# Kernel optimization log

Measured on AMD Instinct MI355X. Metric: run time of the kernel, lower is better.

Reference implementation:

```python
import jax, jax.numpy as jnp
import numpy as np

R = 32  # voxel resolution

def leaky(x):
    return jnp.where(x > 0, x, 0.1 * x)

def bn(x, gamma, beta, axes, eps=1e-4):
    mu = jnp.mean(x, axis=axes, keepdims=True)
    var = jnp.var(x, axis=axes, keepdims=True)
    shape = [1] * x.ndim
    shape[1] = x.shape[1]
    g = gamma.reshape(shape)
    b = beta.reshape(shape)
    return (x - mu) * jax.lax.rsqrt(var + eps) * g + b

def voxelize(features, coords, r):
    # features: (B, C, N), coords: (B, 3, N)
    B, C, N = features.shape
    mean = jnp.mean(coords, axis=2, keepdims=True)
    norm = (coords - mean + 1.0) / 2.0 * r
    norm = jnp.clip(norm, 0.0, r - 1.0)            # (B, 3, N) continuous voxel coords
    vox = jnp.round(norm).astype(jnp.int32)
    flat = (vox[:, 0] * r + vox[:, 1]) * r + vox[:, 2]      # (B, N)
    seg = (flat + jnp.arange(B, dtype=jnp.int32)[:, None] * (r ** 3)).reshape(-1)
    data = features.transpose(0, 2, 1).reshape(B * N, C)
    sums = jax.ops.segment_sum(data, seg, num_segments=B * r ** 3)
    cnt = jax.ops.segment_sum(jnp.ones((B * N,), data.dtype), seg, num_segments=B * r ** 3)
    avg = sums / jnp.maximum(cnt, 1.0)[:, None]
    grid = avg.reshape(B, r, r, r, C).transpose(0, 4, 1, 2, 3)  # (B, C, r, r, r)
    return grid, norm

def trilinear_devoxelize(grid, norm, r):
    # grid: (B, C, r, r, r), norm: (B, 3, N) in [0, r-1]
    B, C = grid.shape[:2]
    N = norm.shape[2]
    lo = jnp.floor(norm).astype(jnp.int32)
    frac = norm - lo.astype(norm.dtype)
    hi = jnp.minimum(lo + 1, r - 1)
    gf = grid.reshape(B, C, r ** 3)
    out = jnp.zeros((B, C, N), grid.dtype)
    for dx in (0, 1):
        for dy in (0, 1):
            for dz in (0, 1):
                ix = hi[:, 0] if dx else lo[:, 0]
                iy = hi[:, 1] if dy else lo[:, 1]
                iz = hi[:, 2] if dz else lo[:, 2]
                wx = frac[:, 0] if dx else 1.0 - frac[:, 0]
                wy = frac[:, 1] if dy else 1.0 - frac[:, 1]
                wz = frac[:, 2] if dz else 1.0 - frac[:, 2]
                idx = (ix * r + iy) * r + iz                    # (B, N)
                g = jnp.take_along_axis(gf, idx[:, None, :], axis=2)  # (B, C, N)
                out = out + g * (wx * wy * wz)[:, None, :]
    return out

def conv3d(x, w, b):
    y = jax.lax.conv_general_dilated(
        x, w, window_strides=(1, 1, 1), padding=[(1, 1)] * 3,
        dimension_numbers=('NCDHW', 'OIDHW', 'NCDHW'))
    return y + b[None, :, None, None, None]

def setup_inputs() -> dict:
    key = jax.random.key(0)
    ks = jax.random.split(key, 8)
    B, Cin, Cout, N = 8, 64, 64, 32768
    s1 = 1.0 / np.sqrt(Cin * 27)
    s2 = 1.0 / np.sqrt(Cout * 27)
    return {
        'features': jax.random.normal(ks[0], (B, Cin, N), jnp.float32),
        'coords': jax.random.normal(ks[1], (B, 3, N), jnp.float32),
        'conv1_w': jax.random.normal(ks[2], (Cout, Cin, 3, 3, 3), jnp.float32) * s1,
        'conv1_b': jnp.zeros((Cout,), jnp.float32),
        'bn1_g': jnp.ones((Cout,), jnp.float32),
        'bn1_b': jnp.zeros((Cout,), jnp.float32),
        'conv2_w': jax.random.normal(ks[3], (Cout, Cout, 3, 3, 3), jnp.float32) * s2,
        'conv2_b': jnp.zeros((Cout,), jnp.float32),
        'bn2_g': jnp.ones((Cout,), jnp.float32),
        'bn2_b': jnp.zeros((Cout,), jnp.float32),
        'mlp_w': jax.random.normal(ks[4], (Cout, Cin), jnp.float32) / np.sqrt(Cin),
        'mlp_b': jnp.zeros((Cout,), jnp.float32),
        'bnp_g': jnp.ones((Cout,), jnp.float32),
        'bnp_b': jnp.zeros((Cout,), jnp.float32),
    }

def reference(features, coords, conv1_w, conv1_b, bn1_g, bn1_b,
              conv2_w, conv2_b, bn2_g, bn2_b, mlp_w, mlp_b, bnp_g, bnp_b):
    grid, norm = voxelize(features, coords, R)
    v = leaky(bn(conv3d(grid, conv1_w, conv1_b), bn1_g, bn1_b, (0, 2, 3, 4)))
    v = leaky(bn(conv3d(v, conv2_w, conv2_b), bn2_g, bn2_b, (0, 2, 3, 4)))
    sampled = trilinear_devoxelize(v, norm, R)                 # (B, Cout, N)
    p = jnp.einsum('oi,bin->bon', mlp_w, features) + mlp_b[None, :, None]
    p = leaky(bn(p, bnp_g, bnp_b, (0, 2)))
    fused = sampled + p
    return fused, v
```

## Files before the change

### kernel.cpp

```cpp
#include <hip/hip_runtime.h>
#include <hip/hip_bf16.h>

#define BB 8
#define CC 64
#define NPTS 32768
#define RR 32
#define RV 32768
#define MTOT (BB*RV)
#define EPSV 1e-4f

#define OFF_BUFA 0u
#define OFF_BUFB 16777216u
#define OFF_WB1  25165824u
#define OFF_WB2  25221120u
#define OFF_ZG   25276416u
#define OFF_BASE 25276480u
#define OFF_AUX  25800768u
#define OFF_CELL 25801024u
#define OFF_CNT  26063168u
#define OFF_MEAN 26325312u
#define OFF_PART1 26325504u
#define OFF_PART2 26456576u
#define OFF_SCL1 26587648u
#define OFF_SFT1 26587712u
#define OFF_SCL2 26587776u
#define OFF_SFT2 26587840u
#define OFF_WM   26587904u
#define OFF_PARTP 26590208u
#define OFF_SCLP 27114496u
#define OFF_SFTP 27114560u
#define OFF_NORM 33554432u

typedef __attribute__((ext_vector_type(8))) __bf16 bf16x8;
typedef __attribute__((ext_vector_type(8))) unsigned short u16x8;
typedef __attribute__((ext_vector_type(4))) float f32x4;

__device__ __forceinline__ float b2f(ushort u) {
    union { unsigned u; float f; } x; x.u = ((unsigned)u) << 16; return x.f;
}
__device__ __forceinline__ ushort f2b(float f) {
    __hip_bfloat16 h = __float2bfloat16(f);
    return *reinterpret_cast<ushort*>(&h);
}

__global__ void k_coord_mean(const float* __restrict__ coords, float* __restrict__ mean) {
    int ba = blockIdx.x >> 3, ch = blockIdx.x & 7;
    const float* src = coords + (size_t)ba * NPTS + ch * 4096;
    float s = 0.f;
    for (int i = threadIdx.x; i < 4096; i += 256) s += src[i];
    __shared__ float red[256];
    red[threadIdx.x] = s; __syncthreads();
    for (int w = 128; w > 0; w >>= 1) {
        if (threadIdx.x < w) red[threadIdx.x] += red[threadIdx.x + w];
        __syncthreads();
    }
    if (threadIdx.x == 0) atomicAdd(&mean[ba], red[0]);
}

__global__ void k_cellid(const float* __restrict__ coords, const float* __restrict__ mean,
                         float* __restrict__ norm, int* __restrict__ cellid,
                         unsigned* __restrict__ cnt) {
    int idx = blockIdx.x * 256 + threadIdx.x;
    int b = idx >> 15, n = idx & (NPTS - 1);
    int flat = 0;
    #pragma unroll
    for (int a = 0; a < 3; ++a) {
        float c = coords[((size_t)(b * 3 + a)) * NPTS + n];
        float nm = (c - mean[b * 3 + a] * (1.0f / NPTS) + 1.0f) * (0.5f * RR);
        nm = fminf(fmaxf(nm, 0.0f), (float)(RR - 1));
        norm[((size_t)(b * 3 + a)) * NPTS + n] = nm;
        flat = flat * RR + (int)rintf(nm);
    }
    int cell = b * RV + flat;
    cellid[idx] = cell;
    atomicAdd(&cnt[cell], 1u);
}

__global__ void k_scan1(const unsigned* __restrict__ cnt, unsigned* __restrict__ base,
                        unsigned* __restrict__ aux) {
    int tid = threadIdx.x;
    int c0 = blockIdx.x * 1024 + tid * 4;
    unsigned v0 = cnt[c0], v1 = cnt[c0 + 1], v2 = cnt[c0 + 2], v3 = cnt[c0 + 3];
    unsigned tot = v0 + v1 + v2 + v3;
    __shared__ unsigned sc[256];
    sc[tid] = tot; __syncthreads();
    for (int off = 1; off < 256; off <<= 1) {
        unsigned t = (tid >= off) ? sc[tid - off] : 0u;
        __syncthreads();
        sc[tid] += t;
        __syncthreads();
    }
    unsigned excl = sc[tid] - tot;
    base[c0] = excl;
    base[c0 + 1] = excl + v0;
    base[c0 + 2] = excl + v0 + v1;
    base[c0 + 3] = excl + v0 + v1 + v2;
    if (tid == 255) aux[blockIdx.x] = sc[255];
}

__global__ void k_scan2(unsigned* __restrict__ aux) {
    int tid = threadIdx.x;
    unsigned own = aux[tid];
    __shared__ unsigned sc[256];
    sc[tid] = own; __syncthreads();
    for (int off = 1; off < 256; off <<= 1) {
        unsigned t = (tid >= off) ? sc[tid - off] : 0u;
        __syncthreads();
        sc[tid] += t;
        __syncthreads();
    }
    aux[tid] = sc[tid] - own;
}

__global__ void k_scan3(unsigned* __restrict__ base, const unsigned* __restrict__ aux) {
    int i = blockIdx.x * 256 + threadIdx.x;
    base[i] += aux[i >> 10];
}

__global__ __launch_bounds__(256) void k_scatfeat(
    const float* __restrict__ feats, const int* __restrict__ cellid,
    unsigned* __restrict__ base, ushort* __restrict__ fsort,
    const ushort* __restrict__ wmb, const float* __restrict__ mbias,
    ushort* __restrict__ pb, float* __restrict__ partp) {
    __shared__ float t[64 * 65];
    __shared__ unsigned spos[64];
    __shared__ float sf[512];
    int b = blockIdx.x >> 9;
    int n0 = (blockIdx.x & 511) * 64;
    int tid = threadIdx.x;
    #pragma unroll
    for (int k = 0; k < 4; ++k) {
        int li = k * 256 + tid;
        int c = li >> 4, n4 = (li & 15) * 4;
        float4 v = *reinterpret_cast<const float4*>(
            &feats[((size_t)(b * 64 + c)) * NPTS + n0 + n4]);
        t[c * 65 + n4 + 0] = v.x;
        t[c * 65 + n4 + 1] = v.y;
        t[c * 65 + n4 + 2] = v.z;
        t[c * 65 + n4 + 3] = v.w;
    }
    if (tid < 64) {
        int cell = cellid[(b << 15) + n0 + tid];
        spos[tid] = atomicAdd(&base[cell], 1u);
    }
    __syncthreads();
    #pragma unroll
    for (int it = 0; it < 2; ++it) {
        int pl = it * 32 + (tid >> 3);
        int j = tid & 7;
        unsigned pos = spos[pl];
        u16x8 v;
        #pragma unroll
        for (int k = 0; k < 8; ++k) v[k] = f2b(t[(j * 8 + k) * 65 + pl]);
        *reinterpret_cast<u16x8*>(fsort + (((size_t)pos) << 6) + j * 8) = v;
    }
    int w = tid >> 6, l = tid & 63;
    int nl = l & 15, kg = l >> 4;
    bf16x8 Af[2];
    #pragma unroll
    for (int ks = 0; ks < 2; ++ks) {
        union { u16x8 u; bf16x8 h; } cv;
        #pragma unroll
        for (int j = 0; j < 8; ++j)
            cv.u[j] = f2b(t[(ks * 32 + kg * 8 + j) * 65 + w * 16 + nl]);
        Af[ks] = cv.h;
    }
    f32x4 acc[4];
    #pragma unroll
    for (int cb = 0; cb < 4; ++cb) acc[cb] = (f32x4){0.f, 0.f, 0.f, 0.f};
    #pragma unroll
    for (int ks = 0; ks < 2; ++ks)
        #pragma unroll
        for (int cb = 0; cb < 4; ++cb) {
            bf16x8 Bf = *reinterpret_cast<const bf16x8*>(wmb + (cb * 16 + nl) * 64 + ks * 32 + kg * 8);
            acc[cb] = __builtin_amdgcn_mfma_f32_16x16x32_bf16(Af[ks], Bf, acc[cb], 0, 0, 0);
        }
    float ss[4] = {0.f, 0.f, 0.f, 0.f}, qq[4] = {0.f, 0.f, 0.f, 0.f};
    #pragma unroll
    for (int cb = 0; cb < 4; ++cb) {
        float bsv = mbias[cb * 16 + nl];
        #pragma unroll
        for (int r = 0; r < 4; ++r) {
            float yv = acc[cb][r] + bsv;
            int pt = w * 16 + kg * 4 + r;
            pb[(((size_t)((b << 15) + n0 + pt)) << 6) + cb * 16 + nl] = f2b(yv);
            ss[cb] += yv; qq[cb] += yv * yv;
        }
    }
    #pragma unroll
    for (int cb = 0; cb < 4; ++cb) {
        ss[cb] += __shfl_xor(ss[cb], 16); ss[cb] += __shfl_xor(ss[cb], 32);
        qq[cb] += __shfl_xor(qq[cb], 16); qq[cb] += __shfl_xor(qq[cb], 32);
    }
    if (l < 16) {
        #pragma unroll
        for (int cb = 0; cb < 4; ++cb) {
            sf[w * 128 + cb * 16 + nl] = ss[cb];
            sf[w * 128 + 64 + cb * 16 + nl] = qq[cb];
        }
    }
    __syncthreads();
    if (tid < 128)
        partp[(size_t)tid * 4096 + blockIdx.x] =
            sf[tid] + sf[128 + tid] + sf[256 + tid] + sf[384 + tid];
}

__global__ __launch_bounds__(256) void k_gather(
    const ushort* __restrict__ fsort, const unsigned* __restrict__ base,
    const unsigned* __restrict__ cnt, __hip_bfloat16* __restrict__ xb) {
    int cell = blockIdx.x * 4 + (threadIdx.x >> 6);
    int lane = threadIdx.x & 63;
    unsigned n = cnt[cell];
    unsigned start = base[cell] - n;
    const ushort* rows = fsort + (((size_t)start) << 6) + lane;
    float acc = 0.f;
    unsigned i = 0;
    for (; i + 8 <= n; i += 8) {
        float f0 = b2f(rows[((size_t)(i + 0)) << 6]);
        float f1 = b2f(rows[((size_t)(i + 1)) << 6]);
        float f2 = b2f(rows[((size_t)(i + 2)) << 6]);
        float f3 = b2f(rows[((size_t)(i + 3)) << 6]);
        float f4 = b2f(rows[((size_t)(i + 4)) << 6]);
        float f5 = b2f(rows[((size_t)(i + 5)) << 6]);
        float f6 = b2f(rows[((size_t)(i + 6)) << 6]);
        float f7 = b2f(rows[((size_t)(i + 7)) << 6]);
        acc += ((f0 + f1) + (f2 + f3)) + ((f4 + f5) + (f6 + f7));
    }
    for (; i < n; ++i) acc += b2f(rows[((size_t)i) << 6]);
    float inv = (n > 0) ? (1.0f / (float)n) : 0.f;
    xb[((size_t)cell << 6) + lane] = __float2bfloat16(acc * inv);
}

__global__ void k_wb(const float* __restrict__ w, __hip_bfloat16* __restrict__ wb) {
    int i = blockIdx.x * 256 + threadIdx.x;
    if (i >= CC * CC * 27) return;
    int tap = i % 27, t = i / 27;
    int ci = t & 63, co = t >> 6;
    int half = ci >> 5;
    wb[(((size_t)((half * 27 + tap) * 64 + co)) << 5) + (ci & 31)] = __float2bfloat16(w[i]);
}

__global__ void k_wm(const float* __restrict__ w, ushort* __restrict__ wmb) {
    int i = blockIdx.x * 256 + threadIdx.x;
    if (i < 4096) wmb[i] = f2b(w[i]);
}

template<int MODE>
__global__ __launch_bounds__(512, 4) void k_conv_mfma(
    const ushort* __restrict__ src, const ushort* __restrict__ wb,
    const float* __restrict__ bias, const float* __restrict__ scl,
    const float* __restrict__ sft, ushort* __restrict__ y,
    float* __restrict__ part, const ushort* __restrict__ zg) {
    __shared__ __align__(16) char sh[64000 + 16384];
    char* wsh = sh + 64000;
    int tid = threadIdx.x;
    int lane = tid & 63, wid = tid >> 6;
    int tile = ((blockIdx.x & 7) << 6) | (blockIdx.x >> 3);
    int twi = tile & 3, thi = (tile >> 2) & 3;
    int tdi = (tile >> 4) & 3, b = tile >> 6;
    int d0 = tdi * 8, h0 = thi * 8, w0 = twi * 8;

    auto stage_wgt = [&](int half, int g) {
        const ushort* wgrp = wb + (((half * 27 + g * 2)) << 11);
        char* wdst = wsh + (g & 1) * 8192;
        int c = (wid << 6) + lane;
        int row = c >> 2, off = c & 3;
        const ushort* gsrc = wgrp + (((row << 2) + (off ^ (row & 3))) << 3);
        __builtin_amdgcn_global_load_lds(
            (const __attribute__((address_space(1))) void*)gsrc,
            (__attribute__((address_space(3))) void*)(wdst + (wid << 10)), 16, 0, 0);
    };

    auto stage_halo = [&](int half) {
        float sc8[8], sf8[8];
        if (MODE == 1) {
            int c0 = half * 32 + (lane & 3) * 8;
            #pragma unroll
            for (int j = 0; j < 8; ++j) { sc8[j] = scl[c0 + j]; sf8[j] = sft[c0 + j]; }
        }
        #pragma unroll
        for (int it = 0; it < 8; ++it) {
            int idx = it * 8 + wid;
            int c = (idx << 6) + lane;
            if (c < 4000) {
                int row = c >> 2, off = c & 3;
                int dz = row / 100, rem = row - dz * 100;
                int hz = rem / 10, wz = rem - hz * 10;
                int gd = d0 - 1 + dz, gh = h0 - 1 + hz, gw = w0 - 1 + wz;
                bool inb = ((unsigned)gd < 32u) && ((unsigned)gh < 32u) && ((unsigned)gw < 32u);
                size_t vbase = (((size_t)((b << 15) | (gd << 10) | (gh << 5) | gw)) << 6) + half * 32;
                if (MODE == 0) {
                    int soff = off ^ (row & 3);
                    const ushort* gsrc = inb ? src + vbase + soff * 8 : zg;
                    __builtin_amdgcn_global_load_lds(
                        (const __attribute__((address_space(1))) void*)gsrc,
                        (__attribute__((address_space(3))) void*)(sh + (idx << 10)), 16, 0, 0);
                } else {
                    u16x8 v = {0, 0, 0, 0, 0, 0, 0, 0};
                    if (inb) {
                        v = *reinterpret_cast<const u16x8*>(src + vbase + off * 8);
                        #pragma unroll
                        for (int j = 0; j < 8; ++j) {
                            float f = fmaf(b2f(v[j]), sc8[j], sf8[j]);
                            f = f > 0.f ? f : 0.1f * f;
                            v[j] = f2b(f);
                        }
                    }
                    *reinterpret_cast<u16x8*>(sh + (row << 6) + ((off ^ (row & 3)) << 4)) = v;
                }
            }
        }
    };

    int nl = lane & 15, kg = lane >> 4;
    int rbase = wid * 100 + (nl >> 3) * 10 + (nl & 7);

    f32x4 acc[4][4];
    #pragma unroll
    for (int mi = 0; mi < 4; ++mi)
        #pragma unroll
        for (int cb = 0; cb < 4; ++cb) acc[mi][cb] = (f32x4){0.f, 0.f, 0.f, 0.f};

    auto compute = [&](int g) {
        const char* wlds = wsh + (g & 1) * 8192;
        #pragma unroll
        for (int tl = 0; tl < 2; ++tl) {
            int t = g * 2 + tl;
            if (t < 27) {
                int kd = t / 9, rm = t - kd * 9;
                int kh = rm / 3, kw = rm - kh * 3;
                int rt = rbase + kd * 100 + kh * 10 + kw;
                bf16x8 a[4];
                #pragma unroll
                for (int mi = 0; mi < 4; ++mi) {
                    int r = rt + mi * 20;
                    a[mi] = *reinterpret_cast<const bf16x8*>(
                        sh + (r << 6) + ((kg ^ (r & 3)) << 4));
                }
                bf16x8 bf[4];
                #pragma unroll
                for (int cb = 0; cb < 4; ++cb) {
                    int rowb = tl * 64 + cb * 16 + nl;
                    bf[cb] = *reinterpret_cast<const bf16x8*>(
                        wlds + (rowb << 6) + ((kg ^ (rowb & 3)) << 4));
                }
                __builtin_amdgcn_s_setprio(1);
                #pragma unroll
                for (int mi = 0; mi < 4; ++mi)
                    #pragma unroll
                    for (int cb = 0; cb < 4; ++cb)
                        acc[mi][cb] = __builtin_amdgcn_mfma_f32_16x16x32_bf16(
                            a[mi], bf[cb], acc[mi][cb], 0, 0, 0);
                __builtin_amdgcn_s_setprio(0);
            }
        }
    };

    stage_halo(0);
    stage_wgt(0, 0);
    __syncthreads();
    #pragma unroll 1
    for (int g = 0; g < 14; ++g) {
        if (g < 13) stage_wgt(0, g + 1);
        compute(g);
        __syncthreads();
    }
    stage_halo(1);
    stage_wgt(1, 0);
    __syncthreads();
    #pragma unroll 1
    for (int g = 0; g < 14; ++g) {
        if (g < 13) stage_wgt(1, g + 1);
        compute(g);
        __syncthreads();
    }

    int d = d0 + wid;
    float bs[4];
    #pragma unroll
    for (int cb = 0; cb < 4; ++cb) bs[cb] = bias[cb * 16 + nl];
    float ss[4] = {0.f, 0.f, 0.f, 0.f}, qq[4] = {0.f, 0.f, 0.f, 0.f};
    #pragma unroll
    for (int mi = 0; mi < 4; ++mi) {
        int h = h0 + mi * 2 + (kg >> 1);
        int w = w0 + (kg & 1) * 4;
        size_t vox = (size_t)((b << 15) | (d << 10) | (h << 5) | w);
        #pragma unroll
        for (int cb = 0; cb < 4; ++cb) {
            int co = cb * 16 + nl;
            #pragma unroll
            for (int r = 0; r < 4; ++r) {
                float yv = acc[mi][cb][r] + bs[cb];
                y[((vox + r) << 6) + co] = f2b(yv);
                ss[cb] += yv; qq[cb] += yv * yv;
            }
        }
    }
    #pragma unroll
    for (int cb = 0; cb < 4; ++cb) {
        ss[cb] += __shfl_xor(ss[cb], 16); ss[cb] += __shfl_xor(ss[cb], 32);
        qq[cb] += __shfl_xor(qq[cb], 16); qq[cb] += __shfl_xor(qq[cb], 32);
    }
    float* sf2 = (float*)sh;
    __syncthreads();
    if (lane < 16) {
        #pragma unroll
        for (int cb = 0; cb < 4; ++cb) {
            sf2[wid * 128 + cb * 16 + nl] = ss[cb];
            sf2[wid * 128 + 64 + cb * 16 + nl] = qq[cb];
        }
    }
    __syncthreads();
    if (tid < 128) {
        float t = sf2[tid] + sf2[128 + tid] + sf2[256 + tid] + sf2[384 + tid]
                + sf2[512 + tid] + sf2[640 + tid] + sf2[768 + tid] + sf2[896 + tid];
        part[tid * 512 + blockIdx.x] = t;
    }
}

__global__ void k_redbn(const float* __restrict__ part, const float* __restrict__ g,
                        const float* __restrict__ bb, float* __restrict__ scl,
                        float* __restrict__ sft, int cnt) {
    int c = blockIdx.x;
    float s = 0.f, q = 0.f;
    for (int i = threadIdx.x; i < cnt; i += 256) {
        s += part[(size_t)c * cnt + i];
        q += part[(size_t)(64 + c) * cnt + i];
    }
    __shared__ float rs[256], rq[256];
    rs[threadIdx.x] = s; rq[threadIdx.x] = q; __syncthreads();
    for (int w = 128; w > 0; w >>= 1) {
        if (threadIdx.x < w) { rs[threadIdx.x] += rs[threadIdx.x + w]; rq[threadIdx.x] += rq[threadIdx.x + w]; }
        __syncthreads();
    }
    if (threadIdx.x == 0) {
        float mu = rs[0] * (1.0f / MTOT);
        float var = rq[0] * (1.0f / MTOT) - mu * mu;
        float sc = g[c] * rsqrtf(var + EPSV);
        scl[c] = sc; sft[c] = bb[c] - mu * sc;
    }
}

__global__ void k_transpose(const ushort* __restrict__ in, const float* __restrict__ scl,
                            const float* __restrict__ sft, float* __restrict__ out) {
    __shared__ float t[64 * 65];
    size_t base = (size_t)blockIdx.x * 4096;
    int gv0 = blockIdx.x * 64;
    int b = gv0 >> 15;
    int vox0 = gv0 & 32767;
    int tid = threadIdx.x;
    #pragma unroll
    for (int k = 0; k < 2; ++k) {
        int li = k * 256 + tid;
        int vox = li >> 3, c0 = (li & 7) * 8;
        u16x8 v = *reinterpret_cast<const u16x8*>(in + base + vox * 64 + c0);
        #pragma unroll
        for (int j = 0; j < 8; ++j)
            t[(c0 + j) * 65 + vox] = b2f(v[j]);
    }
    __syncthreads();
    #pragma unroll
    for (int k = 0; k < 4; ++k) {
        int li = k * 256 + tid;
        int ch = li >> 4, v4 = (li & 15) * 4;
        float sc = scl[ch], sf = sft[ch];
        float4 o;
        float a0 = fmaf(t[ch * 65 + v4 + 0], sc, sf); o.x = a0 > 0.f ? a0 : 0.1f * a0;
        float a1 = fmaf(t[ch * 65 + v4 + 1], sc, sf); o.y = a1 > 0.f ? a1 : 0.1f * a1;
        float a2 = fmaf(t[ch * 65 + v4 + 2], sc, sf); o.z = a2 > 0.f ? a2 : 0.1f * a2;
        float a3 = fmaf(t[ch * 65 + v4 + 3], sc, sf); o.w = a3 > 0.f ? a3 : 0.1f * a3;
        *reinterpret_cast<float4*>(&out[((size_t)(b * 64 + ch)) * RV + vox0 + v4]) = o;
    }
}

__global__ __launch_bounds__(256) void k_final(
    float* __restrict__ out, const ushort* __restrict__ pbuf,
    const ushort* __restrict__ vraw, const float* __restrict__ norm,
    const float* __restrict__ scl, const float* __restrict__ sft,
    const float* __restrict__ sclp, const float* __restrict__ sftp) {
    __shared__ float smp[64 * 65];
    int b = blockIdx.x >> 9;
    int n0 = (blockIdx.x & 511) * 64;
    int wid = threadIdx.x >> 6, lane = threadIdx.x & 63;
    const ushort* gb = vraw + (((size_t)b) << 15) * CC;
    const float* nrm0 = norm + ((size_t)(b * 3)) * NPTS;
    float sc = scl[lane], sf = sft[lane];
    float scp = sclp[lane], sfp = sftp[lane];

    #pragma unroll 2
    for (int i = 0; i < 16; ++i) {
        int pl = wid * 16 + i;
        int n = n0 + pl;
        float v0 = nrm0[n];
        float v1 = nrm0[NPTS + n];
        float v2 = nrm0[2 * NPTS + n];
        int lx = (int)floorf(v0), ly = (int)floorf(v1), lz = (int)floorf(v2);
        float fx = v0 - (float)lx, fy = v1 - (float)ly, fz = v2 - (float)lz;
        int hx = min(lx + 1, 31), hy = min(ly + 1, 31), hz = min(lz + 1, 31);
        float gx = 1.f - fx, gy = 1.f - fy, gz = 1.f - fz;

        int i000 = ((lx * 32 + ly) * 32 + lz) << 6;
        int i001 = ((lx * 32 + ly) * 32 + hz) << 6;
        int i010 = ((lx * 32 + hy) * 32 + lz) << 6;
        int i011 = ((lx * 32 + hy) * 32 + hz) << 6;
        int i100 = ((hx * 32 + ly) * 32 + lz) << 6;
        int i101 = ((hx * 32 + ly) * 32 + hz) << 6;
        int i110 = ((hx * 32 + hy) * 32 + lz) << 6;
        int i111 = ((hx * 32 + hy) * 32 + hz) << 6;

        float w000 = gx * gy * gz, w001 = gx * gy * fz;
        float w010 = gx * fy * gz, w011 = gx * fy * fz;
        float w100 = fx * gy * gz, w101 = fx * gy * fz;
        float w110 = fx * fy * gz, w111 = fx * fy * fz;

        float r0 = fmaf(b2f(gb[i000 + lane]), sc, sf); r0 = r0 > 0.f ? r0 : 0.1f * r0;
        float r1 = fmaf(b2f(gb[i001 + lane]), sc, sf); r1 = r1 > 0.f ? r1 : 0.1f * r1;
        float r2 = fmaf(b2f(gb[i010 + lane]), sc, sf); r2 = r2 > 0.f ? r2 : 0.1f * r2;
        float r3 = fmaf(b2f(gb[i011 + lane]), sc, sf); r3 = r3 > 0.f ? r3 : 0.1f * r3;
        float r4 = fmaf(b2f(gb[i100 + lane]), sc, sf); r4 = r4 > 0.f ? r4 : 0.1f * r4;
        float r5 = fmaf(b2f(gb[i101 + lane]), sc, sf); r5 = r5 > 0.f ? r5 : 0.1f * r5;
        float r6 = fmaf(b2f(gb[i110 + lane]), sc, sf); r6 = r6 > 0.f ? r6 : 0.1f * r6;
        float r7 = fmaf(b2f(gb[i111 + lane]), sc, sf); r7 = r7 > 0.f ? r7 : 0.1f * r7;

        float s = r0 * w000 + r1 * w001 + r2 * w010 + r3 * w011
                + r4 * w100 + r5 * w101 + r6 * w110 + r7 * w111;

        float pv = fmaf(b2f(pbuf[(((size_t)((b << 15) + n)) << 6) + lane]), scp, sfp);
        pv = pv > 0.f ? pv : 0.1f * pv;
        smp[pl * 65 + lane] = s + pv;
    }
    __syncthreads();

    #pragma unroll 4
    for (int i = 0; i < 16; ++i) {
        int co = i * 4 + wid;
        out[((size_t)(b * 64 + co)) * NPTS + n0 + lane] = smp[lane * 65 + co];
    }
}

extern "C" void kernel_launch(void* const* d_in, const int* in_sizes, int n_in,
                              void* d_out, int out_size, void* d_ws, size_t ws_size,
                              hipStream_t stream) {
    const float* features = (const float*)d_in[0];
    const float* coords   = (const float*)d_in[1];
    const float* conv1_w  = (const float*)d_in[2];
    const float* conv1_b  = (const float*)d_in[3];
    const float* bn1_g    = (const float*)d_in[4];
    const float* bn1_b    = (const float*)d_in[5];
    const float* conv2_w  = (const float*)d_in[6];
    const float* conv2_b  = (const float*)d_in[7];
    const float* bn2_g    = (const float*)d_in[8];
    const float* bn2_b    = (const float*)d_in[9];
    const float* mlp_w    = (const float*)d_in[10];
    const float* mlp_b    = (const float*)d_in[11];
    const float* bnp_g    = (const float*)d_in[12];
    const float* bnp_b    = (const float*)d_in[13];

    float* ws    = (float*)d_ws;
    ushort* fsort  = (ushort*)(ws + OFF_BUFA);
    ushort* y2b    = (ushort*)(ws + OFF_BUFA);
    __hip_bfloat16* xb  = (__hip_bfloat16*)(ws + OFF_BUFB);
    __hip_bfloat16* wb1 = (__hip_bfloat16*)(ws + OFF_WB1);
    __hip_bfloat16* wb2 = (__hip_bfloat16*)(ws + OFF_WB2);
    ushort* zg   = (ushort*)(ws + OFF_ZG);
    unsigned* base    = (unsigned*)(ws + OFF_BASE);
    unsigned* aux     = (unsigned*)(ws + OFF_AUX);
    int* cellid       = (int*)(ws + OFF_CELL);
    unsigned* cnt     = (unsigned*)(ws + OFF_CNT);
    float* mean  = ws + OFF_MEAN;
    float* part1 = ws + OFF_PART1;
    float* part2 = ws + OFF_PART2;
    float* scl1  = ws + OFF_SCL1;
    float* sft1  = ws + OFF_SFT1;
    float* scl2  = ws + OFF_SCL2;
    float* sft2  = ws + OFF_SFT2;
    ushort* wmb  = (ushort*)(ws + OFF_WM);
    float* partp = ws + OFF_PARTP;
    float* sclp  = ws + OFF_SCLP;
    float* sftp  = ws + OFF_SFTP;
    float* nrm   = ws + OFF_NORM;

    float* outF  = (float*)d_out;
    float* outV  = (float*)d_out + (size_t)16777216;
    ushort* y1b  = (ushort*)outV;
    ushort* pbuf = (ushort*)(outV + (size_t)8388608);

    hipMemsetAsync(cnt, 0, 262144 * 4, stream);
    hipMemsetAsync(zg, 0, 256, stream);
    hipMemsetAsync(mean, 0, 24 * 4, stream);

    k_coord_mean<<<192, 256, 0, stream>>>(coords, mean);
    k_cellid<<<1024, 256, 0, stream>>>(coords, mean, nrm, cellid, cnt);
    k_scan1<<<256, 256, 0, stream>>>(cnt, base, aux);
    k_scan2<<<1, 256, 0, stream>>>(aux);
    k_scan3<<<1024, 256, 0, stream>>>(base, aux);

    k_wb<<<432, 256, 0, stream>>>(conv1_w, wb1);
    k_wb<<<432, 256, 0, stream>>>(conv2_w, wb2);
    k_wm<<<16, 256, 0, stream>>>(mlp_w, wmb);

    k_scatfeat<<<4096, 256, 0, stream>>>(features, cellid, base, fsort,
                                         wmb, mlp_b, pbuf, partp);
    k_redbn<<<64, 256, 0, stream>>>(partp, bnp_g, bnp_b, sclp, sftp, 4096);
    k_gather<<<65536, 256, 0, stream>>>(fsort, base, cnt, xb);

    k_conv_mfma<0><<<512, 512, 0, stream>>>((const ushort*)xb, (const ushort*)wb1, conv1_b,
                                            nullptr, nullptr, y1b, part1, zg);
    k_redbn<<<64, 256, 0, stream>>>(part1, bn1_g, bn1_b, scl1, sft1, 512);

    k_conv_mfma<1><<<512, 512, 0, stream>>>(y1b, (const ushort*)wb2, conv2_b,
                                            scl1, sft1, y2b, part2, zg);
    k_redbn<<<64, 256, 0, stream>>>(part2, bn2_g, bn2_b, scl2, sft2, 512);

    k_final<<<4096, 256, 0, stream>>>(outF, pbuf, y2b, nrm, scl2, sft2, sclp, sftp);

    k_transpose<<<4096, 256, 0, stream>>>(y2b, scl2, sft2, outV);
}
```

Before: 354.1 us.

## Merge small launches: fold scan fixup, fuse weight prep, combine final kernels

Drops the scan-fixup kernel by adding the block offset (aux) directly inside the scatter and gather kernels. The three weight-conversion launches become a single prep kernel. The final sampling kernel and the voxel transpose become one 8192-block epilogue. Because both epilogue halves run concurrently, pbuf moves out of the outV region into workspace so the transpose writes cannot clobber it. The aim is fewer launches and idle tails, at the cost of an extra aux load per access.

```diff
diff --git a/kernel.cpp b/kernel.cpp
--- a/kernel.cpp
+++ b/kernel.cpp
@@ -112,14 +112,29 @@
     aux[tid] = sc[tid] - own;
 }
 
-__global__ void k_scan3(unsigned* __restrict__ base, const unsigned* __restrict__ aux) {
-    int i = blockIdx.x * 256 + threadIdx.x;
-    base[i] += aux[i >> 10];
+__global__ void k_prep(const float* __restrict__ w1, const float* __restrict__ w2,
+                       const float* __restrict__ wm, __hip_bfloat16* __restrict__ wb1,
+                       __hip_bfloat16* __restrict__ wb2, ushort* __restrict__ wmb) {
+    int bid = blockIdx.x;
+    if (bid < 864) {
+        const float* w = (bid < 432) ? w1 : w2;
+        __hip_bfloat16* wb = (bid < 432) ? wb1 : wb2;
+        int i = (bid % 432) * 256 + threadIdx.x;
+        if (i >= CC * CC * 27) return;
+        int tap = i % 27, t = i / 27;
+        int ci = t & 63, co = t >> 6;
+        int half = ci >> 5;
+        wb[(((size_t)((half * 27 + tap) * 64 + co)) << 5) + (ci & 31)] = __float2bfloat16(w[i]);
+    } else {
+        int i = (bid - 864) * 256 + threadIdx.x;
+        if (i < 4096) wmb[i] = f2b(wm[i]);
+    }
 }
 
 __global__ __launch_bounds__(256) void k_scatfeat(
     const float* __restrict__ feats, const int* __restrict__ cellid,
-    unsigned* __restrict__ base, ushort* __restrict__ fsort,
+    unsigned* __restrict__ base, const unsigned* __restrict__ aux,
+    ushort* __restrict__ fsort,
     const ushort* __restrict__ wmb, const float* __restrict__ mbias,
     ushort* __restrict__ pb, float* __restrict__ partp) {
     __shared__ float t[64 * 65];
@@ -141,7 +156,7 @@
     }
     if (tid < 64) {
         int cell = cellid[(b << 15) + n0 + tid];
-        spos[tid] = atomicAdd(&base[cell], 1u);
+        spos[tid] = atomicAdd(&base[cell], 1u) + aux[cell >> 10];
     }
     __syncthreads();
     #pragma unroll
@@ -207,11 +222,12 @@
 
 __global__ __launch_bounds__(256) void k_gather(
     const ushort* __restrict__ fsort, const unsigned* __restrict__ base,
-    const unsigned* __restrict__ cnt, __hip_bfloat16* __restrict__ xb) {
+    const unsigned* __restrict__ aux, const unsigned* __restrict__ cnt,
+    __hip_bfloat16* __restrict__ xb) {
     int cell = blockIdx.x * 4 + (threadIdx.x >> 6);
     int lane = threadIdx.x & 63;
     unsigned n = cnt[cell];
-    unsigned start = base[cell] - n;
+    unsigned start = base[cell] - n + aux[cell >> 10];
     const ushort* rows = fsort + (((size_t)start) << 6) + lane;
     float acc = 0.f;
     unsigned i = 0;
@@ -229,20 +245,6 @@
     for (; i < n; ++i) acc += b2f(rows[((size_t)i) << 6]);
     float inv = (n > 0) ? (1.0f / (float)n) : 0.f;
     xb[((size_t)cell << 6) + lane] = __float2bfloat16(acc * inv);
-}
-
-__global__ void k_wb(const float* __restrict__ w, __hip_bfloat16* __restrict__ wb) {
-    int i = blockIdx.x * 256 + threadIdx.x;
-    if (i >= CC * CC * 27) return;
-    int tap = i % 27, t = i / 27;
-    int ci = t & 63, co = t >> 6;
-    int half = ci >> 5;
-    wb[(((size_t)((half * 27 + tap) * 64 + co)) << 5) + (ci & 31)] = __float2bfloat16(w[i]);
-}
-
-__global__ void k_wm(const float* __restrict__ w, ushort* __restrict__ wmb) {
-    int i = blockIdx.x * 256 + threadIdx.x;
-    if (i < 4096) wmb[i] = f2b(w[i]);
 }
 
 template<int MODE>
@@ -441,100 +443,101 @@
     }
 }
 
-__global__ void k_transpose(const ushort* __restrict__ in, const float* __restrict__ scl,
-                            const float* __restrict__ sft, float* __restrict__ out) {
-    __shared__ float t[64 * 65];
-    size_t base = (size_t)blockIdx.x * 4096;
-    int gv0 = blockIdx.x * 64;
-    int b = gv0 >> 15;
-    int vox0 = gv0 & 32767;
-    int tid = threadIdx.x;
-    #pragma unroll
-    for (int k = 0; k < 2; ++k) {
-        int li = k * 256 + tid;
-        int vox = li >> 3, c0 = (li & 7) * 8;
-        u16x8 v = *reinterpret_cast<const u16x8*>(in + base + vox * 64 + c0);
-        #pragma unroll
-        for (int j = 0; j < 8; ++j)
-            t[(c0 + j) * 65 + vox] = b2f(v[j]);
-    }
-    __syncthreads();
-    #pragma unroll
-    for (int k = 0; k < 4; ++k) {
-        int li = k * 256 + tid;
-        int ch = li >> 4, v4 = (li & 15) * 4;
-        float sc = scl[ch], sf = sft[ch];
-        float4 o;
-        float a0 = fmaf(t[ch * 65 + v4 + 0], sc, sf); o.x = a0 > 0.f ? a0 : 0.1f * a0;
-        float a1 = fmaf(t[ch * 65 + v4 + 1], sc, sf); o.y = a1 > 0.f ? a1 : 0.1f * a1;
-        float a2 = fmaf(t[ch * 65 + v4 + 2], sc, sf); o.z = a2 > 0.f ? a2 : 0.1f * a2;
-        float a3 = fmaf(t[ch * 65 + v4 + 3], sc, sf); o.w = a3 > 0.f ? a3 : 0.1f * a3;
-        *reinterpret_cast<float4*>(&out[((size_t)(b * 64 + ch)) * RV + vox0 + v4]) = o;
-    }
-}
-
-__global__ __launch_bounds__(256) void k_final(
-    float* __restrict__ out, const ushort* __restrict__ pbuf,
-    const ushort* __restrict__ vraw, const float* __restrict__ norm,
+__global__ __launch_bounds__(256) void k_epilogue(
+    float* __restrict__ outF, float* __restrict__ outV,
+    const ushort* __restrict__ pbuf, const ushort* __restrict__ vraw,
+    const float* __restrict__ norm,
     const float* __restrict__ scl, const float* __restrict__ sft,
     const float* __restrict__ sclp, const float* __restrict__ sftp) {
     __shared__ float smp[64 * 65];
-    int b = blockIdx.x >> 9;
-    int n0 = (blockIdx.x & 511) * 64;
-    int wid = threadIdx.x >> 6, lane = threadIdx.x & 63;
-    const ushort* gb = vraw + (((size_t)b) << 15) * CC;
-    const float* nrm0 = norm + ((size_t)(b * 3)) * NPTS;
-    float sc = scl[lane], sf = sft[lane];
-    float scp = sclp[lane], sfp = sftp[lane];
-
-    #pragma unroll 2
-    for (int i = 0; i < 16; ++i) {
-        int pl = wid * 16 + i;
-        int n = n0 + pl;
-        float v0 = nrm0[n];
-        float v1 = nrm0[NPTS + n];
-        float v2 = nrm0[2 * NPTS + n];
-        int lx = (int)floorf(v0), ly = (int)floorf(v1), lz = (int)floorf(v2);
-        float fx = v0 - (float)lx, fy = v1 - (float)ly, fz = v2 - (float)lz;
-        int hx = min(lx + 1, 31), hy = min(ly + 1, 31), hz = min(lz + 1, 31);
-        float gx = 1.f - fx, gy = 1.f - fy, gz = 1.f - fz;
-
-        int i000 = ((lx * 32 + ly) * 32 + lz) << 6;
-        int i001 = ((lx * 32 + ly) * 32 + hz) << 6;
-        int i010 = ((lx * 32 + hy) * 32 + lz) << 6;
-        int i011 = ((lx * 32 + hy) * 32 + hz) << 6;
-        int i100 = ((hx * 32 + ly) * 32 + lz) << 6;
-        int i101 = ((hx * 32 + ly) * 32 + hz) << 6;
-        int i110 = ((hx * 32 + hy) * 32 + lz) << 6;
-        int i111 = ((hx * 32 + hy) * 32 + hz) << 6;
-
-        float w000 = gx * gy * gz, w001 = gx * gy * fz;
-        float w010 = gx * fy * gz, w011 = gx * fy * fz;
-        float w100 = fx * gy * gz, w101 = fx * gy * fz;
-        float w110 = fx * fy * gz, w111 = fx * fy * fz;
-
-        float r0 = fmaf(b2f(gb[i000 + lane]), sc, sf); r0 = r0 > 0.f ? r0 : 0.1f * r0;
-        float r1 = fmaf(b2f(gb[i001 + lane]), sc, sf); r1 = r1 > 0.f ? r1 : 0.1f * r1;
-        float r2 = fmaf(b2f(gb[i010 + lane]), sc, sf); r2 = r2 > 0.f ? r2 : 0.1f * r2;
-        float r3 = fmaf(b2f(gb[i011 + lane]), sc, sf); r3 = r3 > 0.f ? r3 : 0.1f * r3;
-        float r4 = fmaf(b2f(gb[i100 + lane]), sc, sf); r4 = r4 > 0.f ? r4 : 0.1f * r4;
-        float r5 = fmaf(b2f(gb[i101 + lane]), sc, sf); r5 = r5 > 0.f ? r5 : 0.1f * r5;
-        float r6 = fmaf(b2f(gb[i110 + lane]), sc, sf); r6 = r6 > 0.f ? r6 : 0.1f * r6;
-        float r7 = fmaf(b2f(gb[i111 + lane]), sc, sf); r7 = r7 > 0.f ? r7 : 0.1f * r7;
-
-        float s = r0 * w000 + r1 * w001 + r2 * w010 + r3 * w011
-                + r4 * w100 + r5 * w101 + r6 * w110 + r7 * w111;
-
-        float pv = fmaf(b2f(pbuf[(((size_t)((b << 15) + n)) << 6) + lane]), scp, sfp);
-        pv = pv > 0.f ? pv : 0.1f * pv;
-        smp[pl * 65 + lane] = s + pv;
-    }
-    __syncthreads();
-
-    #pragma unroll 4
-    for (int i = 0; i < 16; ++i) {
-        int co = i * 4 + wid;
-        out[((size_t)(b * 64 + co)) * NPTS + n0 + lane] = smp[lane * 65 + co];
+    int tid = threadIdx.x;
+    if (blockIdx.x < 4096) {
+        int bid = blockIdx.x;
+        int b = bid >> 9;
+        int n0 = (bid & 511) * 64;
+        int wid = tid >> 6, lane = tid & 63;
+        const ushort* gb = vraw + (((size_t)b) << 15) * CC;
+        const float* nrm0 = norm + ((size_t)(b * 3)) * NPTS;
+        float sc = scl[lane], sf = sft[lane];
+        float scp = sclp[lane], sfp = sftp[lane];
+
+        #pragma unroll 2
+        for (int i = 0; i < 16; ++i) {
+            int pl = wid * 16 + i;
+            int n = n0 + pl;
+            float v0 = nrm0[n];
+            float v1 = nrm0[NPTS + n];
+            float v2 = nrm0[2 * NPTS + n];
+            int lx = (int)floorf(v0), ly = (int)floorf(v1), lz = (int)floorf(v2);
+            float fx = v0 - (float)lx, fy = v1 - (float)ly, fz = v2 - (float)lz;
+            int hx = min(lx + 1, 31), hy = min(ly + 1, 31), hz = min(lz + 1, 31);
+            float gx = 1.f - fx, gy = 1.f - fy, gz = 1.f - fz;
+
+            int i000 = ((lx * 32 + ly) * 32 + lz) << 6;
+            int i001 = ((lx * 32 + ly) * 32 + hz) << 6;
+            int i010 = ((lx * 32 + hy) * 32 + lz) << 6;
+            int i011 = ((lx * 32 + hy) * 32 + hz) << 6;
+            int i100 = ((hx * 32 + ly) * 32 + lz) << 6;
+            int i101 = ((hx * 32 + ly) * 32 + hz) << 6;
+            int i110 = ((hx * 32 + hy) * 32 + lz) << 6;
+            int i111 = ((hx * 32 + hy) * 32 + hz) << 6;
+
+            float w000 = gx * gy * gz, w001 = gx * gy * fz;
+            float w010 = gx * fy * gz, w011 = gx * fy * fz;
+            float w100 = fx * gy * gz, w101 = fx * gy * fz;
+            float w110 = fx * fy * gz, w111 = fx * fy * fz;
+
+            float r0 = fmaf(b2f(gb[i000 + lane]), sc, sf); r0 = r0 > 0.f ? r0 : 0.1f * r0;
+            float r1 = fmaf(b2f(gb[i001 + lane]), sc, sf); r1 = r1 > 0.f ? r1 : 0.1f * r1;
+            float r2 = fmaf(b2f(gb[i010 + lane]), sc, sf); r2 = r2 > 0.f ? r2 : 0.1f * r2;
+            float r3 = fmaf(b2f(gb[i011 + lane]), sc, sf); r3 = r3 > 0.f ? r3 : 0.1f * r3;
+            float r4 = fmaf(b2f(gb[i100 + lane]), sc, sf); r4 = r4 > 0.f ? r4 : 0.1f * r4;
+            float r5 = fmaf(b2f(gb[i101 + lane]), sc, sf); r5 = r5 > 0.f ? r5 : 0.1f * r5;
+            float r6 = fmaf(b2f(gb[i110 + lane]), sc, sf); r6 = r6 > 0.f ? r6 : 0.1f * r6;
+            float r7 = fmaf(b2f(gb[i111 + lane]), sc, sf); r7 = r7 > 0.f ? r7 : 0.1f * r7;
+
+            float s = r0 * w000 + r1 * w001 + r2 * w010 + r3 * w011
+                    + r4 * w100 + r5 * w101 + r6 * w110 + r7 * w111;
+
+            float pv = fmaf(b2f(pbuf[(((size_t)((b << 15) + n)) << 6) + lane]), scp, sfp);
+            pv = pv > 0.f ? pv : 0.1f * pv;
+            smp[pl * 65 + lane] = s + pv;
+        }
+        __syncthreads();
+
+        #pragma unroll 4
+        for (int i = 0; i < 16; ++i) {
+            int co = i * 4 + wid;
+            outF[((size_t)(b * 64 + co)) * NPTS + n0 + lane] = smp[lane * 65 + co];
+        }
+    } else {
+        int bid = blockIdx.x - 4096;
+        size_t base = (size_t)bid * 4096;
+        int gv0 = bid * 64;
+        int b = gv0 >> 15;
+        int vox0 = gv0 & 32767;
+        #pragma unroll
+        for (int k = 0; k < 2; ++k) {
+            int li = k * 256 + tid;
+            int vox = li >> 3, c0 = (li & 7) * 8;
+            u16x8 v = *reinterpret_cast<const u16x8*>(vraw + base + vox * 64 + c0);
+            #pragma unroll
+            for (int j = 0; j < 8; ++j)
+                smp[(c0 + j) * 65 + vox] = b2f(v[j]);
+        }
+        __syncthreads();
+        #pragma unroll
+        for (int k = 0; k < 4; ++k) {
+            int li = k * 256 + tid;
+            int ch = li >> 4, v4 = (li & 15) * 4;
+            float sc = scl[ch], sf = sft[ch];
+            float4 o;
+            float a0 = fmaf(smp[ch * 65 + v4 + 0], sc, sf); o.x = a0 > 0.f ? a0 : 0.1f * a0;
+            float a1 = fmaf(smp[ch * 65 + v4 + 1], sc, sf); o.y = a1 > 0.f ? a1 : 0.1f * a1;
+            float a2 = fmaf(smp[ch * 65 + v4 + 2], sc, sf); o.z = a2 > 0.f ? a2 : 0.1f * a2;
+            float a3 = fmaf(smp[ch * 65 + v4 + 3], sc, sf); o.w = a3 > 0.f ? a3 : 0.1f * a3;
+            *reinterpret_cast<float4*>(&outV[((size_t)(b * 64 + ch)) * RV + vox0 + v4]) = o;
+        }
     }
 }
 
@@ -559,6 +562,7 @@
     float* ws    = (float*)d_ws;
     ushort* fsort  = (ushort*)(ws + OFF_BUFA);
     ushort* y2b    = (ushort*)(ws + OFF_BUFA);
+    ushort* pbuf   = (ushort*)(ws + OFF_BUFA) + (size_t)16777216;
     __hip_bfloat16* xb  = (__hip_bfloat16*)(ws + OFF_BUFB);
     __hip_bfloat16* wb1 = (__hip_bfloat16*)(ws + OFF_WB1);
     __hip_bfloat16* wb2 = (__hip_bfloat16*)(ws + OFF_WB2);
@@ -583,7 +587,6 @@
     float* outF  = (float*)d_out;
     float* outV  = (float*)d_out + (size_t)16777216;
     ushort* y1b  = (ushort*)outV;
-    ushort* pbuf = (ushort*)(outV + (size_t)8388608);
 
     hipMemsetAsync(cnt, 0, 262144 * 4, stream);
     hipMemsetAsync(zg, 0, 256, stream);
@@ -593,16 +596,13 @@
     k_cellid<<<1024, 256, 0, stream>>>(coords, mean, nrm, cellid, cnt);
     k_scan1<<<256, 256, 0, stream>>>(cnt, base, aux);
     k_scan2<<<1, 256, 0, stream>>>(aux);
-    k_scan3<<<1024, 256, 0, stream>>>(base, aux);
-
-    k_wb<<<432, 256, 0, stream>>>(conv1_w, wb1);
-    k_wb<<<432, 256, 0, stream>>>(conv2_w, wb2);
-    k_wm<<<16, 256, 0, stream>>>(mlp_w, wmb);
-
-    k_scatfeat<<<4096, 256, 0, stream>>>(features, cellid, base, fsort,
+
+    k_prep<<<880, 256, 0, stream>>>(conv1_w, conv2_w, mlp_w, wb1, wb2, wmb);
+
+    k_scatfeat<<<4096, 256, 0, stream>>>(features, cellid, base, aux, fsort,
                                          wmb, mlp_b, pbuf, partp);
     k_redbn<<<64, 256, 0, stream>>>(partp, bnp_g, bnp_b, sclp, sftp, 4096);
-    k_gather<<<65536, 256, 0, stream>>>(fsort, base, cnt, xb);
+    k_gather<<<65536, 256, 0, stream>>>(fsort, base, aux, cnt, xb);
 
     k_conv_mfma<0><<<512, 512, 0, stream>>>((const ushort*)xb, (const ushort*)wb1, conv1_b,
                                             nullptr, nullptr, y1b, part1, zg);
@@ -612,7 +612,6 @@
                                             scl1, sft1, y2b, part2, zg);
     k_redbn<<<64, 256, 0, stream>>>(part2, bn2_g, bn2_b, scl2, sft2, 512);
 
-    k_final<<<4096, 256, 0, stream>>>(outF, pbuf, y2b, nrm, scl2, sft2, sclp, sftp);
-
-    k_transpose<<<4096, 256, 0, stream>>>(y2b, scl2, sft2, outV);
-}
+    k_epilogue<<<8192, 256, 0, stream>>>(outF, outV, pbuf, y2b, nrm,
+                                         scl2, sft2, sclp, sftp);
+}
```

Result: faster. 338.7 us (-4.3%).
